# Performance work log

Hardware: AMD Instinct MI355X
Metric: run time of the kernel (lower is better)

The kernel has to match this reference:

```python
import jax, jax.numpy as jnp
import numpy as np

D = 256; NH = 8; HD = D // NH; NL = 4; NP = 4; DFF = 1024; NLAYERS = 6; BS = 2
SHAPES = np.array([[100, 100], [50, 50], [25, 25], [13, 13]], dtype=np.int64)  # (H, W) per level
S = int((SHAPES[:, 0] * SHAPES[:, 1]).sum())  # 13294 flattened tokens


def setup_inputs() -> dict:
    key = jax.random.key(0)
    ks = jax.random.split(key, 12)
    p = lambda k, sh, sc: jax.random.normal(k, sh, jnp.float32) * sc
    return {
        "src": p(ks[0], (BS, S, D), 1.0),
        "pos": p(ks[1], (BS, S, D), 0.1),
        "valid_ratios": 0.5 + 0.5 * jax.random.uniform(ks[2], (BS, NL, 2), jnp.float32),
        "W_off": p(ks[3], (NLAYERS, D, NH * NL * NP * 2), 0.01),
        "b_off": jnp.zeros((NLAYERS, NH * NL * NP * 2), jnp.float32),
        "W_attn": p(ks[4], (NLAYERS, D, NH * NL * NP), 0.02),
        "b_attn": jnp.zeros((NLAYERS, NH * NL * NP), jnp.float32),
        "W_val": p(ks[5], (NLAYERS, D, D), 0.02),
        "b_val": jnp.zeros((NLAYERS, D), jnp.float32),
        "W_out": p(ks[6], (NLAYERS, D, D), 0.02),
        "b_out": jnp.zeros((NLAYERS, D), jnp.float32),
        "g1": jnp.ones((NLAYERS, D), jnp.float32),
        "be1": jnp.zeros((NLAYERS, D), jnp.float32),
        "W_ff1": p(ks[7], (NLAYERS, D, DFF), 0.02),
        "b_ff1": jnp.zeros((NLAYERS, DFF), jnp.float32),
        "W_ff2": p(ks[8], (NLAYERS, DFF, D), 0.02),
        "b_ff2": jnp.zeros((NLAYERS, D), jnp.float32),
        "g2": jnp.ones((NLAYERS, D), jnp.float32),
        "be2": jnp.zeros((NLAYERS, D), jnp.float32),
    }


def layer_norm(x, g, b, eps=1e-5):
    m = x.mean(-1, keepdims=True)
    v = jnp.var(x, axis=-1, keepdims=True)
    return (x - m) * jax.lax.rsqrt(v + eps) * g + b


def get_reference_points(valid_ratios):
    """Faithful port of DeformableTransformerEncoder.get_reference_points."""
    refs = []
    for lvl in range(NL):
        Hh, Ww = int(SHAPES[lvl, 0]), int(SHAPES[lvl, 1])
        ry, rx = jnp.meshgrid(jnp.linspace(0.5, Hh - 0.5, Hh, dtype=jnp.float32),
                              jnp.linspace(0.5, Ww - 0.5, Ww, dtype=jnp.float32), indexing="ij")
        ry = ry.reshape(-1)[None] / (valid_ratios[:, None, lvl, 1] * Hh)
        rx = rx.reshape(-1)[None] / (valid_ratios[:, None, lvl, 0] * Ww)
        refs.append(jnp.stack((rx, ry), -1))
    rp = jnp.concatenate(refs, 1)                       # [bs, S, 2]
    return rp[:, :, None] * valid_ratios[:, None]       # [bs, S, NL, 2]


def ms_deform_sample(value, locs, attn):
    """Multi-scale deformable attention core (grid_sample bilinear, zeros padding,
    align_corners=False).
    value: [bs,S,NH,HD]  locs: [bs,S,NH,NL,NP,2]  attn: [bs,S,NH,NL,NP]"""
    bs = value.shape[0]
    out = jnp.zeros((bs, NH, S, HD), value.dtype)
    start = 0
    for lvl in range(NL):
        Hh, Ww = int(SHAPES[lvl, 0]), int(SHAPES[lvl, 1])
        v = value[:, start:start + Hh * Ww].transpose(0, 2, 1, 3)  # [bs,NH,HW,HD]
        start += Hh * Ww
        loc = locs[:, :, :, lvl].transpose(0, 2, 1, 3, 4)           # [bs,NH,S,NP,2]
        x = loc[..., 0] * Ww - 0.5
        y = loc[..., 1] * Hh - 0.5
        x0 = jnp.floor(x)
        y0 = jnp.floor(y)
        wx1 = x - x0
        wy1 = y - y0
        acc = jnp.zeros((bs, NH, S, NP, HD), value.dtype)
        for dy in (0, 1):
            for dx in (0, 1):
                xi = x0 + dx
                yi = y0 + dy
                w = (wx1 if dx else 1.0 - wx1) * (wy1 if dy else 1.0 - wy1)
                valid = (xi >= 0) & (xi < Ww) & (yi >= 0) & (yi < Hh)
                idx = (jnp.clip(yi, 0, Hh - 1) * Ww + jnp.clip(xi, 0, Ww - 1)).astype(jnp.int32)
                g = jnp.take_along_axis(v, idx.reshape(bs, NH, S * NP, 1), axis=2)
                g = g.reshape(bs, NH, S, NP, HD)
                acc = acc + g * (w * valid)[..., None]
        out = out + (acc * attn[:, :, :, lvl].transpose(0, 2, 1, 3)[..., None]).sum(3)
    return out  # [bs,NH,S,HD]


def encoder_layer(src, ref, pos, params):
    (Wo, bo, Wa, ba, Wv, bv, Wout, bout, g1, be1, Wf1, bf1, Wf2, bf2, g2, be2) = params
    q = src + pos  # with_pos_embed
    value = (src @ Wv + bv).reshape(BS, S, NH, HD)
    off = (q @ Wo + bo).reshape(BS, S, NH, NL, NP, 2)
    attn = jax.nn.softmax((q @ Wa + ba).reshape(BS, S, NH, NL * NP), -1).reshape(BS, S, NH, NL, NP)
    # offset normalizer is (W, H) per level
    norm = jnp.asarray(np.stack([SHAPES[:, 1], SHAPES[:, 0]], -1), jnp.float32)  # [NL,2]
    locs = ref[:, :, None, :, None, :] + off / norm[None, None, None, :, None, :]
    sampled = ms_deform_sample(value, locs, attn)                    # [bs,NH,S,HD]
    src2 = sampled.transpose(0, 2, 1, 3).reshape(BS, S, D) @ Wout + bout
    src = layer_norm(src + src2, g1, be1)
    ff = jax.nn.relu(src @ Wf1 + bf1) @ Wf2 + bf2
    return layer_norm(src + ff, g2, be2)


def reference(src, pos, valid_ratios, W_off, b_off, W_attn, b_attn, W_val, b_val,
              W_out, b_out, g1, be1, W_ff1, b_ff1, W_ff2, b_ff2, g2, be2):
    ref = get_reference_points(valid_ratios)
    out = src
    for l in range(NLAYERS):
        params = (W_off[l], b_off[l], W_attn[l], b_attn[l], W_val[l], b_val[l],
                  W_out[l], b_out[l], g1[l], be1[l], W_ff1[l], b_ff1[l],
                  W_ff2[l], b_ff2[l], g2[l], be2[l])
        out = encoder_layer(out, ref, pos, params)
    return out
```

## Files before the change

### kernel.cpp

```cpp
#include <hip/hip_runtime.h>
#include <math.h>
#include <stdint.h>

#define D_MODEL 256
#define NH 8
#define HD 32
#define NL 4
#define NP 4
#define DFF 1024
#define NLAYERS 6
#define BS 2
#define S_TOK 13294
#define MTOT (BS * S_TOK)
#define MPAD 26624

typedef unsigned short u16;
typedef __attribute__((ext_vector_type(8))) __bf16 bf16x8;
typedef __attribute__((ext_vector_type(4))) float f32x4;

#define AS1 __attribute__((address_space(1)))
#define AS3 __attribute__((address_space(3)))

__device__ inline u16 bf16_rne(float f) {
    union { float f; uint32_t u; } v; v.f = f;
    uint32_t u = v.u;
    return (u16)((u + 0x7FFFu + ((u >> 16) & 1u)) >> 16);
}

#define WT_L 753664
#define WT_OA2 0
#define WT_OV 98304
#define WT_OOUT 163840
#define WT_OF1 229376
#define WT_OF2 491520

__global__ void wprep_kernel(const float* __restrict__ Wv, const float* __restrict__ Wo,
                             const float* __restrict__ Wa, const float* __restrict__ Wout,
                             const float* __restrict__ Wf1, const float* __restrict__ Wf2,
                             u16* __restrict__ dst)
{
    int idx = blockIdx.x * blockDim.x + threadIdx.x;
    if (idx >= NLAYERS * WT_L) return;
    int l = idx / WT_L;
    int r = idx - l * WT_L;
    float val;
    if (r < WT_OV) {
        int n = r >> 8, k = r & 255;
        if (n < 256) val = Wo[(size_t)l * 65536 + k * 256 + n];
        else         val = Wa[(size_t)l * 32768 + k * 128 + (n - 256)];
    } else if (r < WT_OOUT) {
        int sr = r - WT_OV; int n = sr >> 8, k = sr & 255;
        val = Wv[(size_t)l * 65536 + k * 256 + n];
    } else if (r < WT_OF1) {
        int sr = r - WT_OOUT; int n = sr >> 8, k = sr & 255;
        val = Wout[(size_t)l * 65536 + k * 256 + n];
    } else if (r < WT_OF2) {
        int sr = r - WT_OF1; int n = sr >> 8, k = sr & 255;
        val = Wf1[(size_t)l * 262144 + k * 1024 + n];
    } else {
        int sr = r - WT_OF2; int n = sr >> 10, k = sr & 1023;
        val = Wf2[(size_t)l * 262144 + k * 256 + n];
    }
    dst[(size_t)l * WT_L + r] = bf16_rne(val);
}

__global__ void refpoints_kernel(const float* __restrict__ vr, float* __restrict__ ref)
{
    int t = blockIdx.x * blockDim.x + threadIdx.x;
    if (t >= MTOT) return;
    int b = t / S_TOK;
    int s = t - b * S_TOK;
    int lvl, W, H, start;
    if (s < 10000)      { lvl = 0; W = 100; H = 100; start = 0; }
    else if (s < 12500) { lvl = 1; W = 50;  H = 50;  start = 10000; }
    else if (s < 13125) { lvl = 2; W = 25;  H = 25;  start = 12500; }
    else                { lvl = 3; W = 13;  H = 13;  start = 13125; }
    int wi = s - start;
    int y = wi / W;
    int x = wi - y * W;
    float rx = (x + 0.5f) / (vr[(b * NL + lvl) * 2 + 0] * (float)W);
    float ry = (y + 0.5f) / (vr[(b * NL + lvl) * 2 + 1] * (float)H);
#pragma unroll
    for (int l2 = 0; l2 < NL; l2++) {
        ref[((size_t)t * NL + l2) * 2 + 0] = rx * vr[(b * NL + l2) * 2 + 0];
        ref[((size_t)t * NL + l2) * 2 + 1] = ry * vr[(b * NL + l2) * 2 + 1];
    }
}

__global__ void conv0_kernel(const float* __restrict__ src, const float* __restrict__ pos,
                             u16* __restrict__ Xb, u16* __restrict__ Qb)
{
    int t = blockIdx.x * blockDim.x + threadIdx.x;
    if (t >= MTOT * 64) return;
    float4 s = ((const float4*)src)[t];
    float4 p = ((const float4*)pos)[t];
    ushort4 a, q;
    a.x = bf16_rne(s.x); a.y = bf16_rne(s.y); a.z = bf16_rne(s.z); a.w = bf16_rne(s.w);
    q.x = bf16_rne(s.x + p.x); q.y = bf16_rne(s.y + p.y);
    q.z = bf16_rne(s.z + p.z); q.w = bf16_rne(s.w + p.w);
    ((ushort4*)Xb)[t] = a;
    ((ushort4*)Qb)[t] = q;
}

template<int MODE>
__global__ __launch_bounds__(256) void gemm_bf16(
    const u16* __restrict__ Aq, const u16* __restrict__ Ax,
    const u16* __restrict__ Bt,
    const float* __restrict__ bias, const float* __restrict__ bias2,
    const float* __restrict__ bias3,
    void* __restrict__ C0, void* __restrict__ C1, void* __restrict__ C2,
    int N, int K)
{
    __shared__ __align__(16) u16 As[128 * 32];
    __shared__ __align__(16) u16 Bs[128 * 32];

    const int tid = threadIdx.x;
    const int wid = tid >> 6;
    const int lane = tid & 63;

    const int nwg = gridDim.x * gridDim.y;
    const int bid = blockIdx.y * gridDim.x + blockIdx.x;
    const int q = nwg >> 3, rr = nwg & 7;
    const int xcd = bid & 7, cidx = bid >> 3;
    const int wg = (xcd < rr ? xcd * (q + 1) : rr * (q + 1) + (xcd - rr) * q) + cidx;
    const int m0 = (wg / gridDim.x) * 128;
    const int n0 = (wg % gridDim.x) * 128;
    const int wr = wid >> 1, wc = wid & 1;

    f32x4 acc[4][4] = {};

    const u16* Ause = (MODE == 4 && n0 >= 384) ? Ax : Aq;
    const u16* a0 = Ause + (size_t)(m0 + (tid >> 2)) * K + (tid & 3) * 8;
    const u16* b0 = Bt + (size_t)(n0 + (tid >> 2)) * K + (tid & 3) * 8;
    u16* asb = As + wid * 512;
    u16* bsb = Bs + wid * 512;

    const int ko = (lane >> 4) * 8;
    const int rsel = lane & 15;

    for (int k0 = 0; k0 < K; k0 += 32) {
        __builtin_amdgcn_global_load_lds((AS1 void*)(a0 + k0), (AS3 void*)(asb), 16, 0, 0);
        __builtin_amdgcn_global_load_lds((AS1 void*)(a0 + (size_t)64 * K + k0),
                                         (AS3 void*)(asb + 2048), 16, 0, 0);
        __builtin_amdgcn_global_load_lds((AS1 void*)(b0 + k0), (AS3 void*)(bsb), 16, 0, 0);
        __builtin_amdgcn_global_load_lds((AS1 void*)(b0 + (size_t)64 * K + k0),
                                         (AS3 void*)(bsb + 2048), 16, 0, 0);
        __syncthreads();

        bf16x8 af[4], bfr[4];
#pragma unroll
        for (int i = 0; i < 4; i++) {
            af[i]  = *reinterpret_cast<const bf16x8*>(&As[(wr * 64 + i * 16 + rsel) * 32 + ko]);
            bfr[i] = *reinterpret_cast<const bf16x8*>(&Bs[(wc * 64 + i * 16 + rsel) * 32 + ko]);
        }
#pragma unroll
        for (int i = 0; i < 4; i++)
#pragma unroll
            for (int j = 0; j < 4; j++)
                acc[i][j] = __builtin_amdgcn_mfma_f32_16x16x32_bf16(af[i], bfr[j], acc[i][j], 0, 0, 0);
        __syncthreads();
    }

#pragma unroll
    for (int j = 0; j < 4; j++) {
        int col = n0 + wc * 64 + j * 16 + rsel;
        float bv;
        if (MODE == 4) bv = (n0 < 256) ? bias[col] : (n0 == 256) ? bias2[col - 256] : bias3[col - 384];
        else bv = bias[col];
#pragma unroll
        for (int i = 0; i < 4; i++) {
            int rbase = m0 + wr * 64 + i * 16 + (lane >> 4) * 4;
#pragma unroll
            for (int r2 = 0; r2 < 4; r2++) {
                int gm = rbase + r2;
                float v = acc[i][j][r2] + bv;
                if (MODE == 2) {
                    v = fmaxf(v, 0.f);
                    ((u16*)C0)[(size_t)gm * N + col] = bf16_rne(v);
                } else {
                    if (n0 < 256)       ((float*)C0)[(size_t)gm * 256 + col] = v;
                    else if (n0 == 256) ((float*)C1)[(size_t)gm * 128 + col - 256] = v;
                    else                ((u16*)C2)[(size_t)gm * 256 + col - 384] = bf16_rne(v);
                }
            }
        }
    }
}

template<int LNMODE>
__global__ __launch_bounds__(256) void gemm_ln(
    const u16* __restrict__ A, const u16* __restrict__ Bt,
    const float* __restrict__ bias,
    const float* __restrict__ Xres, const float* __restrict__ g,
    const float* __restrict__ be, const float* __restrict__ pos,
    float* __restrict__ dstf, u16* __restrict__ dstb, u16* __restrict__ dstq,
    int K, int Mguard)
{
    __shared__ __align__(16) u16 As[64 * 32];
    __shared__ __align__(16) u16 Bs[256 * 32];
    __shared__ float redS[64][4], redQ[64][4], mrow[64], irow[64];

    const int tid = threadIdx.x;
    const int wc = tid >> 6;
    const int lane = tid & 63;

    const int nwg = gridDim.x;
    const int q = nwg >> 3;
    const int wg = (blockIdx.x & 7) * q + (blockIdx.x >> 3);
    const int m0 = wg * 64;

    f32x4 acc[4][4] = {};

    const u16* a0 = A + (size_t)(m0 + (tid >> 2)) * K + (tid & 3) * 8;
    const u16* b0 = Bt + (size_t)(tid >> 2) * K + (tid & 3) * 8;
    u16* asb = As + wc * 512;
    u16* bsb = Bs + wc * 512;

    const int gsel = lane >> 4;
    const int rsel = lane & 15;
    const int ko = gsel * 8;

    for (int k0 = 0; k0 < K; k0 += 32) {
        __builtin_amdgcn_global_load_lds((AS1 void*)(a0 + k0), (AS3 void*)(asb), 16, 0, 0);
#pragma unroll
        for (int ii = 0; ii < 4; ii++)
            __builtin_amdgcn_global_load_lds((AS1 void*)(b0 + (size_t)ii * 64 * K + k0),
                                             (AS3 void*)(bsb + ii * 2048), 16, 0, 0);
        __syncthreads();

        bf16x8 af[4], bfr[4];
#pragma unroll
        for (int i = 0; i < 4; i++) {
            af[i]  = *reinterpret_cast<const bf16x8*>(&As[(i * 16 + rsel) * 32 + ko]);
            bfr[i] = *reinterpret_cast<const bf16x8*>(&Bs[(wc * 64 + i * 16 + rsel) * 32 + ko]);
        }
#pragma unroll
        for (int i = 0; i < 4; i++)
#pragma unroll
            for (int j = 0; j < 4; j++)
                acc[i][j] = __builtin_amdgcn_mfma_f32_16x16x32_bf16(af[i], bfr[j], acc[i][j], 0, 0, 0);
        __syncthreads();
    }

    float bias_j[4], g_j[4], be_j[4];
#pragma unroll
    for (int j = 0; j < 4; j++) {
        int col = wc * 64 + j * 16 + rsel;
        bias_j[j] = bias[col]; g_j[j] = g[col]; be_j[j] = be[col];
    }

#pragma unroll
    for (int i = 0; i < 4; i++)
#pragma unroll
    for (int r = 0; r < 4; r++) {
        int row = i * 16 + gsel * 4 + r;
        int grow = m0 + row;
        float s = 0.f, qq = 0.f;
#pragma unroll
        for (int j = 0; j < 4; j++) {
            int col = wc * 64 + j * 16 + rsel;
            float xr = (grow < MTOT) ? Xres[(size_t)grow * 256 + col] : 0.f;
            float v = acc[i][j][r] + bias_j[j] + xr;
            acc[i][j][r] = v;
            s += v; qq += v * v;
        }
#pragma unroll
        for (int m = 1; m <= 8; m <<= 1) {
            s += __shfl_xor(s, m, 64);
            qq += __shfl_xor(qq, m, 64);
        }
        if (rsel == 0) { redS[row][wc] = s; redQ[row][wc] = qq; }
    }
    __syncthreads();
    if (tid < 64) {
        float s  = redS[tid][0] + redS[tid][1] + redS[tid][2] + redS[tid][3];
        float qq = redQ[tid][0] + redQ[tid][1] + redQ[tid][2] + redQ[tid][3];
        float mean = s * (1.f / 256.f);
        float var  = qq * (1.f / 256.f) - mean * mean;
        mrow[tid] = mean;
        irow[tid] = rsqrtf(var + 1e-5f);
    }
    __syncthreads();

#pragma unroll
    for (int i = 0; i < 4; i++)
#pragma unroll
    for (int r = 0; r < 4; r++) {
        int row = i * 16 + gsel * 4 + r;
        int grow = m0 + row;
        if (grow >= Mguard) continue;
        float mean = mrow[row], inv = irow[row];
#pragma unroll
        for (int j = 0; j < 4; j++) {
            int col = wc * 64 + j * 16 + rsel;
            float y = (acc[i][j][r] - mean) * inv * g_j[j] + be_j[j];
            dstf[(size_t)grow * 256 + col] = y;
            dstb[(size_t)grow * 256 + col] = bf16_rne(y);
            if (LNMODE == 2) {
                float pv = (grow < MTOT) ? pos[(size_t)grow * 256 + col] : 0.f;
                dstq[(size_t)grow * 256 + col] = bf16_rne(y + pv);
            }
        }
    }
}

__global__ __launch_bounds__(256) void msdeform_kernel(
    const u16* __restrict__ value, const float* __restrict__ off,
    const float* __restrict__ logits, const float* __restrict__ ref,
    u16* __restrict__ out)
{
    const int total = MTOT * NH * 4;
    const int Q = 415, R = 4;
    int bid = blockIdx.x;
    int xcd = bid & 7, cidx = bid >> 3;
    int wg = (xcd < R ? xcd * (Q + 1) : R * (Q + 1) + (xcd - R) * Q) + cidx;
    int t = wg * 256 + (int)threadIdx.x;
    if (t >= total) return;
    int c8 = t & 3;
    int h  = (t >> 2) & 7;
    int bs = t >> 5;
    int b  = (bs >= S_TOK) ? 1 : 0;

    const int Ws[4] = {100, 50, 25, 13};
    const int Hs[4] = {100, 50, 25, 13};
    const int st[4] = {0, 10000, 12500, 13125};

    const float* offp = off    + ((size_t)bs * NH + h) * 32;
    const float* lgp  = logits + ((size_t)bs * NH + h) * 16;
    const float* refp = ref    + (size_t)bs * NL * 2;

    float lw[16];
    {
        float4 a0 = ((const float4*)lgp)[0];
        float4 a1 = ((const float4*)lgp)[1];
        float4 a2 = ((const float4*)lgp)[2];
        float4 a3 = ((const float4*)lgp)[3];
        lw[0]=a0.x; lw[1]=a0.y; lw[2]=a0.z; lw[3]=a0.w;
        lw[4]=a1.x; lw[5]=a1.y; lw[6]=a1.z; lw[7]=a1.w;
        lw[8]=a2.x; lw[9]=a2.y; lw[10]=a2.z; lw[11]=a2.w;
        lw[12]=a3.x; lw[13]=a3.y; lw[14]=a3.z; lw[15]=a3.w;
        float mx = lw[0];
#pragma unroll
        for (int i = 1; i < 16; i++) mx = fmaxf(mx, lw[i]);
        float s = 0.f;
#pragma unroll
        for (int i = 0; i < 16; i++) { lw[i] = __expf(lw[i] - mx); s += lw[i]; }
        float inv = 1.f / s;
#pragma unroll
        for (int i = 0; i < 16; i++) lw[i] *= inv;
    }

    float acc[8] = {};

#pragma unroll
    for (int l = 0; l < NL; l++) {
        const int W = Ws[l], H = Hs[l];
        const u16* vbase = value + ((size_t)b * S_TOK + st[l]) * D_MODEL + h * HD + c8 * 8;
        const float fW = (float)W, fH = (float)H;
        const float rxw = fmaf(refp[l * 2 + 0], fW, -0.5f);
        const float ryh = fmaf(refp[l * 2 + 1], fH, -0.5f);
#pragma unroll
        for (int p = 0; p < NP; p++) {
            float x = rxw + offp[l * 8 + p * 2 + 0];
            float y = ryh + offp[l * 8 + p * 2 + 1];
            float a = lw[l * 4 + p];
            float x0f = floorf(x), y0f = floorf(y);
            float wx1 = x - x0f, wy1 = y - y0f;
            float wx0 = 1.f - wx1, wy0 = 1.f - wy1;
            int ix0 = (int)x0f, iy0 = (int)y0f;
#pragma unroll
            for (int dy = 0; dy < 2; dy++) {
                int yi = iy0 + dy;
                if (yi < 0 || yi >= H) continue;
                float wy = dy ? wy1 : wy0;
#pragma unroll
                for (int dx = 0; dx < 2; dx++) {
                    int xi = ix0 + dx;
                    if (xi < 0 || xi >= W) continue;
                    float wgt = (dx ? wx1 : wx0) * wy * a;
                    uint4 gv = *(const uint4*)(vbase + (size_t)(yi * W + xi) * D_MODEL);
                    union { uint32_t q; float f; } lo, hi;
                    lo.q = gv.x << 16; hi.q = gv.x & 0xffff0000u;
                    acc[0] = fmaf(lo.f, wgt, acc[0]); acc[1] = fmaf(hi.f, wgt, acc[1]);
                    lo.q = gv.y << 16; hi.q = gv.y & 0xffff0000u;
                    acc[2] = fmaf(lo.f, wgt, acc[2]); acc[3] = fmaf(hi.f, wgt, acc[3]);
                    lo.q = gv.z << 16; hi.q = gv.z & 0xffff0000u;
                    acc[4] = fmaf(lo.f, wgt, acc[4]); acc[5] = fmaf(hi.f, wgt, acc[5]);
                    lo.q = gv.w << 16; hi.q = gv.w & 0xffff0000u;
                    acc[6] = fmaf(lo.f, wgt, acc[6]); acc[7] = fmaf(hi.f, wgt, acc[7]);
                }
            }
        }
    }
    uint4 o;
    o.x = ((uint32_t)bf16_rne(acc[1]) << 16) | bf16_rne(acc[0]);
    o.y = ((uint32_t)bf16_rne(acc[3]) << 16) | bf16_rne(acc[2]);
    o.z = ((uint32_t)bf16_rne(acc[5]) << 16) | bf16_rne(acc[4]);
    o.w = ((uint32_t)bf16_rne(acc[7]) << 16) | bf16_rne(acc[6]);
    ((uint4*)out)[((size_t)bs * NH + h) * 4 + c8] = o;
}

extern "C" void kernel_launch(void* const* d_in, const int* in_sizes, int n_in,
                              void* d_out, int out_size, void* d_ws, size_t ws_size,
                              hipStream_t stream)
{
    const float* src    = (const float*)d_in[0];
    const float* pos    = (const float*)d_in[1];
    const float* vr     = (const float*)d_in[2];
    const float* W_off  = (const float*)d_in[3];
    const float* b_off  = (const float*)d_in[4];
    const float* W_attn = (const float*)d_in[5];
    const float* b_attn = (const float*)d_in[6];
    const float* W_val  = (const float*)d_in[7];
    const float* b_val  = (const float*)d_in[8];
    const float* W_out  = (const float*)d_in[9];
    const float* b_out  = (const float*)d_in[10];
    const float* g1     = (const float*)d_in[11];
    const float* be1    = (const float*)d_in[12];
    const float* W_ff1  = (const float*)d_in[13];
    const float* b_ff1  = (const float*)d_in[14];
    const float* W_ff2  = (const float*)d_in[15];
    const float* b_ff2  = (const float*)d_in[16];
    const float* g2     = (const float*)d_in[17];
    const float* be2    = (const float*)d_in[18];
    float* out = (float*)d_out;

    uint8_t* wp = (uint8_t*)d_ws;
    auto alloc = [&](size_t bytes) { uint8_t* p = wp; wp += (bytes + 255) & ~(size_t)255; return p; };
    float* refb   = (float*)alloc((size_t)MTOT * 8 * 4);
    float* Ybuf   = (float*)alloc((size_t)MPAD * 256 * 4);
    float* Xf     = (float*)alloc((size_t)MPAD * 256 * 4);
    float* offb   = (float*)alloc((size_t)MPAD * 256 * 4);
    float* attb   = (float*)alloc((size_t)MPAD * 128 * 4);
    u16*   valb16 = (u16*)alloc((size_t)MPAD * 256 * 2);
    uint8_t* slabB = alloc((size_t)MPAD * 256 * 2);
    uint8_t* slabC = alloc((size_t)MPAD * 256 * 2);
    u16* Wt = (u16*)alloc((size_t)NLAYERS * WT_L * 2);

    u16* Xb16   = (u16*)slabB;
    u16* samb16 = (u16*)slabB;
    u16* Qb16   = (u16*)slabC;
    u16* Yb16   = (u16*)slabC;
    u16* ffb16  = (u16*)offb;

    const int GY = MPAD / 128;
    const int GLN = MPAD / 64;
    const int MSD_BLOCKS = (MTOT * NH * 4 + 255) / 256;

    wprep_kernel<<<(NLAYERS * WT_L + 255) / 256, 256, 0, stream>>>(
        W_val, W_off, W_attn, W_out, W_ff1, W_ff2, Wt);
    refpoints_kernel<<<(MTOT + 255) / 256, 256, 0, stream>>>(vr, refb);
    conv0_kernel<<<(MTOT * 64 + 255) / 256, 256, 0, stream>>>(src, pos, Xb16, Qb16);

    for (int l = 0; l < NLAYERS; l++) {
        const float* Xres = (l == 0) ? src : Xf;
        const u16* Wl = Wt + (size_t)l * WT_L;

        gemm_bf16<4><<<dim3(5, GY), 256, 0, stream>>>(
            Qb16, Xb16, Wl + WT_OA2,
            b_off + l * 256, b_attn + l * 128, b_val + l * 256,
            offb, attb, valb16, 640, 256);
        msdeform_kernel<<<MSD_BLOCKS, 256, 0, stream>>>(
            valb16, offb, attb, refb, samb16);
        gemm_ln<1><<<GLN, 256, 0, stream>>>(
            samb16, Wl + WT_OOUT, b_out + l * 256,
            Xres, g1 + l * 256, be1 + l * 256, nullptr,
            Ybuf, Yb16, nullptr, 256, MPAD);
        gemm_bf16<2><<<dim3(8, GY), 256, 0, stream>>>(
            Yb16, nullptr, Wl + WT_OF1, b_ff1 + l * DFF, nullptr, nullptr,
            ffb16, nullptr, nullptr, 1024, 256);
        float* dst = (l == NLAYERS - 1) ? out : Xf;
        int mg = (l == NLAYERS - 1) ? MTOT : MPAD;
        gemm_ln<2><<<GLN, 256, 0, stream>>>(
            ffb16, Wl + WT_OF2, b_ff2 + l * 256,
            Ybuf, g2 + l * 256, be2 + l * 256, pos,
            dst, Xb16, Qb16, 1024, mg);
    }
}
```

Before: 1.270 ms.

## Double-buffer GEMM LDS stages and widen deformable sampling to per-head threads

Both GEMM kernels get two LDS buffers, so the next K-slice's global-to-LDS loads are issued before the MFMAs on the current slice. This lets load latency overlap with compute instead of stalling on a barrier every iteration. The deformable sampling kernel now uses one thread per (token, head) covering all 32 channels instead of four threads of 8 channels each. That removes the fourfold redundant offset, softmax and bilinear-weight computation. The costs are double the LDS footprint, four times fewer sampling threads with more registers each (less latency hiding), and wider per-thread gathers.

```diff
diff --git a/kernel.cpp b/kernel.cpp
--- a/kernel.cpp
+++ b/kernel.cpp
@@ -111,8 +111,8 @@
     void* __restrict__ C0, void* __restrict__ C1, void* __restrict__ C2,
     int N, int K)
 {
-    __shared__ __align__(16) u16 As[128 * 32];
-    __shared__ __align__(16) u16 Bs[128 * 32];
+    __shared__ __align__(16) u16 As[2][128 * 32];
+    __shared__ __align__(16) u16 Bs[2][128 * 32];
 
     const int tid = threadIdx.x;
     const int wid = tid >> 6;
@@ -132,26 +132,34 @@
     const u16* Ause = (MODE == 4 && n0 >= 384) ? Ax : Aq;
     const u16* a0 = Ause + (size_t)(m0 + (tid >> 2)) * K + (tid & 3) * 8;
     const u16* b0 = Bt + (size_t)(n0 + (tid >> 2)) * K + (tid & 3) * 8;
-    u16* asb = As + wid * 512;
-    u16* bsb = Bs + wid * 512;
 
     const int ko = (lane >> 4) * 8;
     const int rsel = lane & 15;
 
+#define GSTAGE(buf, kk) do {                                                        \
+    u16* asb = &As[buf][wid * 512];                                                 \
+    u16* bsb = &Bs[buf][wid * 512];                                                 \
+    __builtin_amdgcn_global_load_lds((AS1 void*)(a0 + (kk)), (AS3 void*)(asb), 16, 0, 0); \
+    __builtin_amdgcn_global_load_lds((AS1 void*)(a0 + (size_t)64 * K + (kk)),       \
+                                     (AS3 void*)(asb + 2048), 16, 0, 0);            \
+    __builtin_amdgcn_global_load_lds((AS1 void*)(b0 + (kk)), (AS3 void*)(bsb), 16, 0, 0); \
+    __builtin_amdgcn_global_load_lds((AS1 void*)(b0 + (size_t)64 * K + (kk)),       \
+                                     (AS3 void*)(bsb + 2048), 16, 0, 0);            \
+} while (0)
+
+    GSTAGE(0, 0);
+    asm volatile("s_waitcnt vmcnt(0)" ::: "memory");
+    __syncthreads();
+
+    int cur = 0;
     for (int k0 = 0; k0 < K; k0 += 32) {
-        __builtin_amdgcn_global_load_lds((AS1 void*)(a0 + k0), (AS3 void*)(asb), 16, 0, 0);
-        __builtin_amdgcn_global_load_lds((AS1 void*)(a0 + (size_t)64 * K + k0),
-                                         (AS3 void*)(asb + 2048), 16, 0, 0);
-        __builtin_amdgcn_global_load_lds((AS1 void*)(b0 + k0), (AS3 void*)(bsb), 16, 0, 0);
-        __builtin_amdgcn_global_load_lds((AS1 void*)(b0 + (size_t)64 * K + k0),
-                                         (AS3 void*)(bsb + 2048), 16, 0, 0);
-        __syncthreads();
+        if (k0 + 32 < K) GSTAGE(cur ^ 1, k0 + 32);
 
         bf16x8 af[4], bfr[4];
 #pragma unroll
         for (int i = 0; i < 4; i++) {
-            af[i]  = *reinterpret_cast<const bf16x8*>(&As[(wr * 64 + i * 16 + rsel) * 32 + ko]);
-            bfr[i] = *reinterpret_cast<const bf16x8*>(&Bs[(wc * 64 + i * 16 + rsel) * 32 + ko]);
+            af[i]  = *reinterpret_cast<const bf16x8*>(&As[cur][(wr * 64 + i * 16 + rsel) * 32 + ko]);
+            bfr[i] = *reinterpret_cast<const bf16x8*>(&Bs[cur][(wc * 64 + i * 16 + rsel) * 32 + ko]);
         }
 #pragma unroll
         for (int i = 0; i < 4; i++)
@@ -159,7 +167,9 @@
             for (int j = 0; j < 4; j++)
                 acc[i][j] = __builtin_amdgcn_mfma_f32_16x16x32_bf16(af[i], bfr[j], acc[i][j], 0, 0, 0);
         __syncthreads();
-    }
+        cur ^= 1;
+    }
+#undef GSTAGE
 
 #pragma unroll
     for (int j = 0; j < 4; j++) {
@@ -196,8 +206,8 @@
     float* __restrict__ dstf, u16* __restrict__ dstb, u16* __restrict__ dstq,
     int K, int Mguard)
 {
-    __shared__ __align__(16) u16 As[64 * 32];
-    __shared__ __align__(16) u16 Bs[256 * 32];
+    __shared__ __align__(16) u16 As[2][64 * 32];
+    __shared__ __align__(16) u16 Bs[2][256 * 32];
     __shared__ float redS[64][4], redQ[64][4], mrow[64], irow[64];
 
     const int tid = threadIdx.x;
@@ -213,26 +223,37 @@
 
     const u16* a0 = A + (size_t)(m0 + (tid >> 2)) * K + (tid & 3) * 8;
     const u16* b0 = Bt + (size_t)(tid >> 2) * K + (tid & 3) * 8;
-    u16* asb = As + wc * 512;
-    u16* bsb = Bs + wc * 512;
 
     const int gsel = lane >> 4;
     const int rsel = lane & 15;
     const int ko = gsel * 8;
 
+#define LSTAGE(buf, kk) do {                                                        \
+    u16* asb = &As[buf][wc * 512];                                                  \
+    u16* bsb = &Bs[buf][wc * 512];                                                  \
+    __builtin_amdgcn_global_load_lds((AS1 void*)(a0 + (kk)), (AS3 void*)(asb), 16, 0, 0); \
+    __builtin_amdgcn_global_load_lds((AS1 void*)(b0 + (kk)), (AS3 void*)(bsb), 16, 0, 0); \
+    __builtin_amdgcn_global_load_lds((AS1 void*)(b0 + (size_t)64 * K + (kk)),       \
+                                     (AS3 void*)(bsb + 2048), 16, 0, 0);            \
+    __builtin_amdgcn_global_load_lds((AS1 void*)(b0 + (size_t)128 * K + (kk)),      \
+                                     (AS3 void*)(bsb + 4096), 16, 0, 0);            \
+    __builtin_amdgcn_global_load_lds((AS1 void*)(b0 + (size_t)192 * K + (kk)),      \
+                                     (AS3 void*)(bsb + 6144), 16, 0, 0);            \
+} while (0)
+
+    LSTAGE(0, 0);
+    asm volatile("s_waitcnt vmcnt(0)" ::: "memory");
+    __syncthreads();
+
+    int cur = 0;
     for (int k0 = 0; k0 < K; k0 += 32) {
-        __builtin_amdgcn_global_load_lds((AS1 void*)(a0 + k0), (AS3 void*)(asb), 16, 0, 0);
-#pragma unroll
-        for (int ii = 0; ii < 4; ii++)
-            __builtin_amdgcn_global_load_lds((AS1 void*)(b0 + (size_t)ii * 64 * K + k0),
-                                             (AS3 void*)(bsb + ii * 2048), 16, 0, 0);
-        __syncthreads();
+        if (k0 + 32 < K) LSTAGE(cur ^ 1, k0 + 32);
 
         bf16x8 af[4], bfr[4];
 #pragma unroll
         for (int i = 0; i < 4; i++) {
-            af[i]  = *reinterpret_cast<const bf16x8*>(&As[(i * 16 + rsel) * 32 + ko]);
-            bfr[i] = *reinterpret_cast<const bf16x8*>(&Bs[(wc * 64 + i * 16 + rsel) * 32 + ko]);
+            af[i]  = *reinterpret_cast<const bf16x8*>(&As[cur][(i * 16 + rsel) * 32 + ko]);
+            bfr[i] = *reinterpret_cast<const bf16x8*>(&Bs[cur][(wc * 64 + i * 16 + rsel) * 32 + ko]);
         }
 #pragma unroll
         for (int i = 0; i < 4; i++)
@@ -240,7 +261,9 @@
             for (int j = 0; j < 4; j++)
                 acc[i][j] = __builtin_amdgcn_mfma_f32_16x16x32_bf16(af[i], bfr[j], acc[i][j], 0, 0, 0);
         __syncthreads();
-    }
+        cur ^= 1;
+    }
+#undef LSTAGE
 
     float bias_j[4], g_j[4], be_j[4];
 #pragma unroll
@@ -309,16 +332,15 @@
     const float* __restrict__ logits, const float* __restrict__ ref,
     u16* __restrict__ out)
 {
-    const int total = MTOT * NH * 4;
-    const int Q = 415, R = 4;
+    const int total = MTOT * NH;
+    const int Q = 103, R = 7;
     int bid = blockIdx.x;
     int xcd = bid & 7, cidx = bid >> 3;
     int wg = (xcd < R ? xcd * (Q + 1) : R * (Q + 1) + (xcd - R) * Q) + cidx;
     int t = wg * 256 + (int)threadIdx.x;
     if (t >= total) return;
-    int c8 = t & 3;
-    int h  = (t >> 2) & 7;
-    int bs = t >> 5;
+    int h  = t & 7;
+    int bs = t >> 3;
     int b  = (bs >= S_TOK) ? 1 : 0;
 
     const int Ws[4] = {100, 50, 25, 13};
@@ -350,12 +372,16 @@
         for (int i = 0; i < 16; i++) lw[i] *= inv;
     }
 
-    float acc[8] = {};
+    float acc[32] = {};
+
+#define UNP(gw, i0, i1) { union { uint32_t qq; float ff; } lo_, hi_;               \
+    lo_.qq = (gw) << 16; hi_.qq = (gw) & 0xffff0000u;                              \
+    acc[i0] = fmaf(lo_.ff, wgt, acc[i0]); acc[i1] = fmaf(hi_.ff, wgt, acc[i1]); }
 
 #pragma unroll
     for (int l = 0; l < NL; l++) {
         const int W = Ws[l], H = Hs[l];
-        const u16* vbase = value + ((size_t)b * S_TOK + st[l]) * D_MODEL + h * HD + c8 * 8;
+        const u16* vbase = value + ((size_t)b * S_TOK + st[l]) * D_MODEL + h * HD;
         const float fW = (float)W, fH = (float)H;
         const float rxw = fmaf(refp[l * 2 + 0], fW, -0.5f);
         const float ryh = fmaf(refp[l * 2 + 1], fH, -0.5f);
@@ -378,26 +404,28 @@
                     int xi = ix0 + dx;
                     if (xi < 0 || xi >= W) continue;
                     float wgt = (dx ? wx1 : wx0) * wy * a;
-                    uint4 gv = *(const uint4*)(vbase + (size_t)(yi * W + xi) * D_MODEL);
-                    union { uint32_t q; float f; } lo, hi;
-                    lo.q = gv.x << 16; hi.q = gv.x & 0xffff0000u;
-                    acc[0] = fmaf(lo.f, wgt, acc[0]); acc[1] = fmaf(hi.f, wgt, acc[1]);
-                    lo.q = gv.y << 16; hi.q = gv.y & 0xffff0000u;
-                    acc[2] = fmaf(lo.f, wgt, acc[2]); acc[3] = fmaf(hi.f, wgt, acc[3]);
-                    lo.q = gv.z << 16; hi.q = gv.z & 0xffff0000u;
-                    acc[4] = fmaf(lo.f, wgt, acc[4]); acc[5] = fmaf(hi.f, wgt, acc[5]);
-                    lo.q = gv.w << 16; hi.q = gv.w & 0xffff0000u;
-                    acc[6] = fmaf(lo.f, wgt, acc[6]); acc[7] = fmaf(hi.f, wgt, acc[7]);
+                    const uint4* vp = (const uint4*)(vbase + (size_t)(yi * W + xi) * D_MODEL);
+                    uint4 g0 = vp[0], g1 = vp[1], g2 = vp[2], g3 = vp[3];
+                    UNP(g0.x, 0, 1)   UNP(g0.y, 2, 3)   UNP(g0.z, 4, 5)   UNP(g0.w, 6, 7)
+                    UNP(g1.x, 8, 9)   UNP(g1.y, 10, 11) UNP(g1.z, 12, 13) UNP(g1.w, 14, 15)
+                    UNP(g2.x, 16, 17) UNP(g2.y, 18, 19) UNP(g2.z, 20, 21) UNP(g2.w, 22, 23)
+                    UNP(g3.x, 24, 25) UNP(g3.y, 26, 27) UNP(g3.z, 28, 29) UNP(g3.w, 30, 31)
                 }
             }
         }
     }
-    uint4 o;
-    o.x = ((uint32_t)bf16_rne(acc[1]) << 16) | bf16_rne(acc[0]);
-    o.y = ((uint32_t)bf16_rne(acc[3]) << 16) | bf16_rne(acc[2]);
-    o.z = ((uint32_t)bf16_rne(acc[5]) << 16) | bf16_rne(acc[4]);
-    o.w = ((uint32_t)bf16_rne(acc[7]) << 16) | bf16_rne(acc[6]);
-    ((uint4*)out)[((size_t)bs * NH + h) * 4 + c8] = o;
+#undef UNP
+
+    uint4* op = (uint4*)(out + ((size_t)bs * NH + h) * HD);
+#pragma unroll
+    for (int w = 0; w < 4; w++) {
+        uint4 o;
+        o.x = ((uint32_t)bf16_rne(acc[w * 8 + 1]) << 16) | bf16_rne(acc[w * 8 + 0]);
+        o.y = ((uint32_t)bf16_rne(acc[w * 8 + 3]) << 16) | bf16_rne(acc[w * 8 + 2]);
+        o.z = ((uint32_t)bf16_rne(acc[w * 8 + 5]) << 16) | bf16_rne(acc[w * 8 + 4]);
+        o.w = ((uint32_t)bf16_rne(acc[w * 8 + 7]) << 16) | bf16_rne(acc[w * 8 + 6]);
+        op[w] = o;
+    }
 }
 
 extern "C" void kernel_launch(void* const* d_in, const int* in_sizes, int n_in,
@@ -445,7 +473,7 @@
 
     const int GY = MPAD / 128;
     const int GLN = MPAD / 64;
-    const int MSD_BLOCKS = (MTOT * NH * 4 + 255) / 256;
+    const int MSD_BLOCKS = (MTOT * NH + 255) / 256;
 
     wprep_kernel<<<(NLAYERS * WT_L + 255) / 256, 256, 0, stream>>>(
         W_val, W_off, W_attn, W_out, W_ff1, W_ff2, Wt);
```

Result: slower. 1.678 ms (+32.2%).
